# Performance work log

Measured on AMD Instinct MI355X. Metric: run time of the kernel, lower is better.

Reference implementation:

```python
import jax, jax.numpy as jnp
import numpy as np

D, E, N, DD, K = 1024, 2048, 16, 64, 4  # d_model, d_inner, d_state, dt_rank, d_conv
B, L = 2, 1024
EPS = 1e-5


def setup_inputs() -> dict:
    key = jax.random.key(0)
    ks = jax.random.split(key, 12)
    f = lambda k, s, scale=0.02: (jax.random.normal(k, s, jnp.float32) * scale)
    return dict(
        resid=jax.random.normal(ks[0], (B, L, D), jnp.float32),
        workplace_h=jnp.zeros((B, E, N), jnp.float32),
        norm_w=jnp.ones((D,), jnp.float32),
        skip_w=f(ks[1], (E, D)),
        in_w=f(ks[2], (E, D)),
        conv_w=f(ks[3], (E, 1, K), 0.2),
        conv_b=jnp.zeros((E,), jnp.float32),
        wd1=f(ks[4], (DD, E)),
        wd2_w=f(ks[5], (E, DD)),
        wd2_b=jnp.zeros((E,), jnp.float32),
        wb=f(ks[6], (N, E)),
        wc=f(ks[7], (N, E)),
        A_log=f(ks[8], (E, N), 1.0),
        W_D=jnp.ones((E,), jnp.float32),
        out_w=f(ks[9], (D, E)),
    )


def reference(resid, workplace_h, norm_w, skip_w, in_w, conv_w, conv_b,
              wd1, wd2_w, wd2_b, wb, wc, A_log, W_D, out_w):
    # RMSNorm
    x = resid * jax.lax.rsqrt(jnp.mean(resid ** 2, -1, keepdims=True) + EPS) * norm_w
    skip = x @ skip_w.T                      # [B,L,E]
    xi = x @ in_w.T                          # [B,L,E]
    # depthwise causal conv1d (torch pads both sides then slices to L; equivalent to left-pad K-1)
    xc = jnp.swapaxes(xi, 1, 2)              # [B,E,L]
    xc = jax.lax.conv_general_dilated(
        xc, conv_w, window_strides=(1,), padding=[(K - 1, 0)],
        feature_group_count=E, dimension_numbers=('NCH', 'OIH', 'NCH'))
    xc = xc + conv_b[None, :, None]
    x2 = jax.nn.silu(jnp.swapaxes(xc, 1, 2))  # [B,L,E]

    A = -jnp.exp(A_log)                       # [E,N]
    delta = jax.nn.softplus((x2 @ wd1.T) @ wd2_w.T + wd2_b)   # [B,L,E]
    A_bar = jnp.exp(delta[..., None] * A)                      # [B,L,E,N]
    Bm = x2 @ wb.T                                             # [B,L,N]
    B_bar = delta[..., None] * Bm[:, :, None, :]               # [B,L,E,N]
    Cm = x2 @ wc.T                                             # [B,L,N]

    def step(h, inp):
        a, b_, xl, cl = inp                   # [B,E,N],[B,E,N],[B,E],[B,N]
        h = a * h + b_ * xl[..., None]
        y = jnp.einsum('ben,bn->be', h, cl)
        return h, y

    h0 = jnp.zeros_like(workplace_h)          # workplace_h is zeroed (h[:] = 0)
    xs = (jnp.swapaxes(A_bar, 0, 1), jnp.swapaxes(B_bar, 0, 1),
          jnp.swapaxes(x2, 0, 1), jnp.swapaxes(Cm, 0, 1))
    _, ys = jax.lax.scan(step, h0, xs)        # ys: [L,B,E]
    y = jnp.swapaxes(ys, 0, 1)                # [B,L,E]

    y = (y + x2 * W_D) * jax.nn.silu(skip)
    return resid + y @ out_w.T
```

## Files before the change

kernel.cpp:

```cpp
#include <hip/hip_runtime.h>
#include <math.h>

#define Dm 1024
#define Em 2048
#define Nm 16
#define DDm 64
#define Bb 2
#define Lm 1024
#define Mrows (Bb*Lm)
#define NCH 32
#define CLEN 32
#define KS 16
#define KSO 4
#define PREPB 26112

typedef __attribute__((ext_vector_type(8))) short bf16x8;
typedef __attribute__((ext_vector_type(4))) float f32x4;
typedef unsigned int u32;
typedef unsigned short u16;

__device__ __forceinline__ u16 f2bf(float f) {
    union { float f; u32 u; } v; v.f = f;
    u32 r = v.u + 0x7fffu + ((v.u >> 16) & 1u);
    return (u16)(r >> 16);
}
__device__ __forceinline__ float bf2f(u16 v) {
    union { u32 u; float f; } t; t.u = ((u32)v) << 16; return t.f;
}

__device__ __forceinline__ void async_copy16(const void* g, void* l) {
    __builtin_amdgcn_global_load_lds(
        (const __attribute__((address_space(1))) u32*)g,
        (__attribute__((address_space(3))) u32*)l,
        16, 0, 0);
}

__global__ __launch_bounds__(256) void prep_rms_kernel(const float* __restrict__ skip_w,
                                                       const float* __restrict__ in_w,
                                                       const float* __restrict__ out_w,
                                                       const float* __restrict__ wd2_w,
                                                       const float* __restrict__ wb,
                                                       const float* __restrict__ wc,
                                                       const float* __restrict__ wd1,
                                                       const float* __restrict__ resid,
                                                       const float* __restrict__ norm_w,
                                                       u16* __restrict__ skip_w_bf,
                                                       u16* __restrict__ in_w_bf,
                                                       u16* __restrict__ out_w_bf,
                                                       u16* __restrict__ wd2_bf,
                                                       u16* __restrict__ wtb,
                                                       u16* __restrict__ x) {
    if (blockIdx.x < PREPB) {
        const int R0 = 2097152, R1 = 4194304, R2 = 6291456, R3 = 6422528, R4 = 6684672;
        int i = blockIdx.x * 256 + threadIdx.x;
        if (i < R0) skip_w_bf[i] = f2bf(skip_w[i]);
        else if (i < R1) in_w_bf[i - R0] = f2bf(in_w[i - R0]);
        else if (i < R2) out_w_bf[i - R1] = f2bf(out_w[i - R1]);
        else if (i < R3) wd2_bf[i - R2] = f2bf(wd2_w[i - R2]);
        else if (i < R4) {
            int j = i - R3;
            int c = j >> 11, k = j & 2047;
            float v = 0.f;
            if (c < 16) v = wb[(size_t)c * Em + k];
            else if (c < 32) v = wc[(size_t)(c - 16) * Em + k];
            else if (c < 96) v = wd1[(size_t)(c - 32) * Em + k];
            wtb[j] = f2bf(v);
        }
        return;
    }
    int row = blockIdx.x - PREPB;
    const float* r = resid + (size_t)row * Dm;
    float s = 0.f;
    for (int i = threadIdx.x; i < Dm; i += 256) { float v = r[i]; s += v * v; }
    __shared__ float red[4];
    for (int off = 32; off; off >>= 1) s += __shfl_down(s, off, 64);
    if ((threadIdx.x & 63) == 0) red[threadIdx.x >> 6] = s;
    __syncthreads();
    if (threadIdx.x == 0) {
        float t = red[0] + red[1] + red[2] + red[3];
        red[0] = rsqrtf(t / (float)Dm + 1e-5f);
    }
    __syncthreads();
    float sc = red[0];
    u16* xo = x + (size_t)row * Dm;
    for (int i = threadIdx.x; i < Dm; i += 256) xo[i] = f2bf(r[i] * sc * norm_w[i]);
}


__global__ __launch_bounds__(256) void gemm_db(const u16* __restrict__ A,
                                               const u16* __restrict__ W,
                                               const float* __restrict__ bias,
                                               float* __restrict__ C,
                                               float* __restrict__ C2, int split,
                                               int M, int N, int lda, int klen, int act) {
    __shared__ __align__(16) u16 As[2][128 * 32];
    __shared__ __align__(16) u16 Ws[2][64 * 32];
    int tid = threadIdx.x;
    int lane = tid & 63, wave = tid >> 6;
    int bm = blockIdx.y * 128, bn = blockIdx.x * 64;
    int kbase = blockIdx.z * klen;
    int lm = lane & 15, lq = lane >> 4;
    int wm = (wave & 1) * 64, wn = (wave >> 1) * 32;

    f32x4 acc[4][2] = {};
    int ldrow = lane >> 2;
    int gchunk = ((lane & 3) ^ ((lane >> 3) & 3)) * 8;
    int rdoff = (lq ^ ((lm >> 1) & 3)) * 8;

    const u16* Arow0 = A + (size_t)(bm + wave * 16 + ldrow) * lda + gchunk;
    const u16* Arow1 = A + (size_t)(bm + 64 + wave * 16 + ldrow) * lda + gchunk;
    const u16* Wrow  = W + (size_t)(bn + wave * 16 + ldrow) * lda + gchunk;
    int ldsA = (wave * 16) * 32;
    int ldsA2 = (64 + wave * 16) * 32;

    int nIter = klen / 32;
    async_copy16(Arow0 + kbase, &As[0][ldsA]);
    async_copy16(Arow1 + kbase, &As[0][ldsA2]);
    async_copy16(Wrow + kbase, &Ws[0][ldsA]);
    __syncthreads();

    for (int it = 0; it < nIter; ++it) {
        int cur = it & 1, nxt = cur ^ 1;
        if (it + 1 < nIter) {
            int k0 = kbase + (it + 1) * 32;
            async_copy16(Arow0 + k0, &As[nxt][ldsA]);
            async_copy16(Arow1 + k0, &As[nxt][ldsA2]);
            async_copy16(Wrow + k0, &Ws[nxt][ldsA]);
        }
        bf16x8 a[4], b[2];
        #pragma unroll
        for (int mi = 0; mi < 4; ++mi)
            a[mi] = *(const bf16x8*)&As[cur][(wm + mi * 16 + lm) * 32 + rdoff];
        #pragma unroll
        for (int nj = 0; nj < 2; ++nj)
            b[nj] = *(const bf16x8*)&Ws[cur][(wn + nj * 16 + lm) * 32 + rdoff];
        #pragma unroll
        for (int mi = 0; mi < 4; ++mi)
            #pragma unroll
            for (int nj = 0; nj < 2; ++nj)
                acc[mi][nj] = __builtin_amdgcn_mfma_f32_16x16x32_bf16(a[mi], b[nj], acc[mi][nj], 0, 0, 0);
        __syncthreads();
    }

    int ldc = C2 ? split : N;
    size_t zoff = (size_t)blockIdx.z * M * ldc;
    #pragma unroll
    for (int nj = 0; nj < 2; ++nj) {
        int col = bn + wn + nj * 16 + lm;
        float bv = bias ? bias[col] : 0.f;
        float* Cp = C; int colw = col;
        if (C2 && col >= split) { Cp = C2; colw = col - split; }
        #pragma unroll
        for (int mi = 0; mi < 4; ++mi) {
            #pragma unroll
            for (int r = 0; r < 4; ++r) {
                int row = bm + wm + mi * 16 + lq * 4 + r;
                float v = acc[mi][nj][r] + bv;
                size_t off = zoff + (size_t)row * ldc + colw;
                if (act == 1) {
                    v = fmaxf(v, 0.f) + __logf(1.f + __expf(-fabsf(v)));
                    Cp[off] = v;
                } else if (act == 2) {
                    ((u16*)Cp)[off] = f2bf(v);
                } else {
                    Cp[off] = v;
                }
            }
        }
    }
}

__global__ __launch_bounds__(256) void out_reduce_kernel(const float* __restrict__ part,
                                                         const float* __restrict__ resid,
                                                         float* __restrict__ out) {
    int idx = blockIdx.x * 256 + threadIdx.x;
    const float4* r4 = (const float4*)resid;
    const float4* p4 = (const float4*)part;
    float4 s = r4[idx];
    const int plane = Mrows * Dm / 4;
    #pragma unroll
    for (int ks = 0; ks < KSO; ++ks) {
        float4 p = p4[(size_t)ks * plane + idx];
        s.x += p.x; s.y += p.y; s.z += p.z; s.w += p.w;
    }
    ((float4*)out)[idx] = s;
}

__global__ __launch_bounds__(256) void small_reduce_kernel(const u16* __restrict__ Cp,
                                                           float* __restrict__ Bm,
                                                           float* __restrict__ Cm,
                                                           u16* __restrict__ d1) {
    int idx = blockIdx.x * 256 + threadIdx.x;
    int row = idx >> 7, col = idx & 127;
    float s = 0.f;
    #pragma unroll
    for (int ks = 0; ks < KS; ++ks) s += bf2f(Cp[(size_t)ks * (Mrows * 128) + idx]);
    if (col < 16) Bm[(size_t)row * 16 + col] = s;
    else if (col < 32) Cm[(size_t)row * 16 + (col - 16)] = s;
    else if (col < 96) d1[(size_t)row * 64 + (col - 32)] = f2bf(s);
}

__global__ __launch_bounds__(256) void conv_silu_kernel(const float* __restrict__ xi,
                                                        const float* __restrict__ cw,
                                                        const float* __restrict__ cb,
                                                        u16* __restrict__ x2b, int total) {
    int idx = blockIdx.x * 256 + threadIdx.x;
    if (idx >= total) return;
    int e = idx & (Em - 1);
    int l = (idx >> 11) & (Lm - 1);
    const float* base = xi + idx;
    float w0 = cw[e * 4 + 0], w1 = cw[e * 4 + 1], w2 = cw[e * 4 + 2], w3 = cw[e * 4 + 3];
    float acc = cb[e];
    if (l >= 3) acc += w0 * base[-3 * Em];
    if (l >= 2) acc += w1 * base[-2 * Em];
    if (l >= 1) acc += w2 * base[-1 * Em];
    acc += w3 * base[0];
    float v = acc / (1.f + __expf(-acc));
    x2b[idx] = f2bf(v);
}

__global__ __launch_bounds__(256) void scan1_kernel(const float* __restrict__ delta,
                                                    const u16* __restrict__ x2b,
                                                    const float* __restrict__ Bm,
                                                    const float* __restrict__ A_log,
                                                    float* __restrict__ h_end,
                                                    float* __restrict__ P) {
    int e = (blockIdx.x & 7) * 256 + threadIdx.x;
    int bc = blockIdx.x >> 3;
    int b = bc & 1, c = bc >> 1;
    float A[16];
    {
        const float4* al = (const float4*)(A_log + e * 16);
        float4 q0 = al[0], q1 = al[1], q2 = al[2], q3 = al[3];
        A[0]=-expf(q0.x); A[1]=-expf(q0.y); A[2]=-expf(q0.z); A[3]=-expf(q0.w);
        A[4]=-expf(q1.x); A[5]=-expf(q1.y); A[6]=-expf(q1.z); A[7]=-expf(q1.w);
        A[8]=-expf(q2.x); A[9]=-expf(q2.y); A[10]=-expf(q2.z); A[11]=-expf(q2.w);
        A[12]=-expf(q3.x); A[13]=-expf(q3.y); A[14]=-expf(q3.z); A[15]=-expf(q3.w);
    }
    float h[16], Pr[16];
    #pragma unroll
    for (int k = 0; k < 16; ++k) { h[k] = 0.f; Pr[k] = 1.f; }

    int l0 = c * CLEN;
    const float* dp = delta + ((size_t)(b * Lm + l0)) * Em + e;
    const u16* xp  = x2b   + ((size_t)(b * Lm + l0)) * Em + e;
    const float* bp = Bm    + ((size_t)(b * Lm + l0)) * Nm;

    float d_n = dp[0], x_n = bf2f(xp[0]);
    float4 b0n = *(const float4*)(bp + 0), b1n = *(const float4*)(bp + 4);
    float4 b2n = *(const float4*)(bp + 8), b3n = *(const float4*)(bp + 12);

    #pragma unroll 1
    for (int l = 0; l < CLEN; ++l) {
        float d = d_n, xv = x_n;
        float4 b0 = b0n, b1 = b1n, b2 = b2n, b3 = b3n;
        if (l < CLEN - 1) {
            d_n = dp[(size_t)(l + 1) * Em]; x_n = bf2f(xp[(size_t)(l + 1) * Em]);
            const float* nb = bp + (size_t)(l + 1) * Nm;
            b0n = *(const float4*)(nb); b1n = *(const float4*)(nb + 4);
            b2n = *(const float4*)(nb + 8); b3n = *(const float4*)(nb + 12);
        }
        float dx = d * xv;
        float bb[16] = {b0.x,b0.y,b0.z,b0.w, b1.x,b1.y,b1.z,b1.w,
                        b2.x,b2.y,b2.z,b2.w, b3.x,b3.y,b3.z,b3.w};
        #pragma unroll
        for (int k = 0; k < 16; ++k) {
            float a = __expf(d * A[k]);
            h[k] = a * h[k] + bb[k] * dx;
            Pr[k] *= a;
        }
    }
    size_t base = (((size_t)c * 2 + b) * 16) * 2048 + e;
    #pragma unroll
    for (int k = 0; k < 16; ++k) {
        h_end[base + k * 2048] = h[k];
        P[base + k * 2048] = Pr[k];
    }
}

__global__ __launch_bounds__(256) void scan2_kernel(float* __restrict__ h_end,
                                                    const float* __restrict__ P) {
    int T = blockIdx.x * 256 + threadIdx.x;
    float hi = 0.f;
    float he_n = h_end[T], p_n = P[T];
    #pragma unroll 1
    for (int c = 0; c < NCH; ++c) {
        float he = he_n, p = p_n;
        if (c < NCH - 1) {
            he_n = h_end[(size_t)(c + 1) * 65536 + T];
            p_n  = P[(size_t)(c + 1) * 65536 + T];
        }
        float hnew = fmaf(p, hi, he);
        h_end[(size_t)c * 65536 + T] = hi;
        hi = hnew;
    }
}

__global__ __launch_bounds__(256) void scan3_kernel(const float* __restrict__ delta,
                                                    const u16* __restrict__ x2b,
                                                    const float* __restrict__ Bm,
                                                    const float* __restrict__ Cm,
                                                    const float* __restrict__ A_log,
                                                    const float* __restrict__ h_init,
                                                    const float* __restrict__ skip,
                                                    const float* __restrict__ W_D,
                                                    u16* __restrict__ yb) {
    int e = (blockIdx.x & 7) * 256 + threadIdx.x;
    int bc = blockIdx.x >> 3;
    int b = bc & 1, c = bc >> 1;
    float A[16];
    {
        const float4* al = (const float4*)(A_log + e * 16);
        float4 q0 = al[0], q1 = al[1], q2 = al[2], q3 = al[3];
        A[0]=-expf(q0.x); A[1]=-expf(q0.y); A[2]=-expf(q0.z); A[3]=-expf(q0.w);
        A[4]=-expf(q1.x); A[5]=-expf(q1.y); A[6]=-expf(q1.z); A[7]=-expf(q1.w);
        A[8]=-expf(q2.x); A[9]=-expf(q2.y); A[10]=-expf(q2.z); A[11]=-expf(q2.w);
        A[12]=-expf(q3.x); A[13]=-expf(q3.y); A[14]=-expf(q3.z); A[15]=-expf(q3.w);
    }
    float h[16];
    {
        size_t base = (((size_t)c * 2 + b) * 16) * 2048 + e;
        #pragma unroll
        for (int k = 0; k < 16; ++k) h[k] = h_init[base + k * 2048];
    }
    float wd = W_D[e];

    int l0 = c * CLEN;
    const float* dp = delta + ((size_t)(b * Lm + l0)) * Em + e;
    const u16* xp  = x2b   + ((size_t)(b * Lm + l0)) * Em + e;
    const float* sp = skip  + ((size_t)(b * Lm + l0)) * Em + e;
    const float* bp = Bm    + ((size_t)(b * Lm + l0)) * Nm;
    const float* cp = Cm    + ((size_t)(b * Lm + l0)) * Nm;
    u16* yp = yb + ((size_t)(b * Lm + l0)) * Em + e;

    float d_n = dp[0], x_n = bf2f(xp[0]), s_n = sp[0];
    float4 b0n = *(const float4*)(bp + 0), b1n = *(const float4*)(bp + 4);
    float4 b2n = *(const float4*)(bp + 8), b3n = *(const float4*)(bp + 12);
    float4 c0n = *(const float4*)(cp + 0), c1n = *(const float4*)(cp + 4);
    float4 c2n = *(const float4*)(cp + 8), c3n = *(const float4*)(cp + 12);

    #pragma unroll 1
    for (int l = 0; l < CLEN; ++l) {
        float d = d_n, xv = x_n, sv = s_n;
        float4 b0 = b0n, b1 = b1n, b2 = b2n, b3 = b3n;
        float4 c0 = c0n, c1 = c1n, c2 = c2n, c3 = c3n;
        if (l < CLEN - 1) {
            d_n = dp[(size_t)(l + 1) * Em]; x_n = bf2f(xp[(size_t)(l + 1) * Em]);
            s_n = sp[(size_t)(l + 1) * Em];
            const float* nb = bp + (size_t)(l + 1) * Nm;
            b0n = *(const float4*)(nb); b1n = *(const float4*)(nb + 4);
            b2n = *(const float4*)(nb + 8); b3n = *(const float4*)(nb + 12);
            const float* nc = cp + (size_t)(l + 1) * Nm;
            c0n = *(const float4*)(nc); c1n = *(const float4*)(nc + 4);
            c2n = *(const float4*)(nc + 8); c3n = *(const float4*)(nc + 12);
        }
        float dx = d * xv;
        float bb[16] = {b0.x,b0.y,b0.z,b0.w, b1.x,b1.y,b1.z,b1.w,
                        b2.x,b2.y,b2.z,b2.w, b3.x,b3.y,b3.z,b3.w};
        float cc[16] = {c0.x,c0.y,c0.z,c0.w, c1.x,c1.y,c1.z,c1.w,
                        c2.x,c2.y,c2.z,c2.w, c3.x,c3.y,c3.z,c3.w};
        float yv = 0.f;
        #pragma unroll
        for (int k = 0; k < 16; ++k) {
            float a = __expf(d * A[k]);
            h[k] = a * h[k] + bb[k] * dx;
            yv += h[k] * cc[k];
        }
        float sig = 1.f / (1.f + __expf(-sv));
        yp[(size_t)l * Em] = f2bf((yv + xv * wd) * (sv * sig));
    }
}

extern "C" void kernel_launch(void* const* d_in, const int* in_sizes, int n_in,
                              void* d_out, int out_size, void* d_ws, size_t ws_size,
                              hipStream_t stream) {
    const float* resid  = (const float*)d_in[0];
    const float* norm_w = (const float*)d_in[2];
    const float* skip_w = (const float*)d_in[3];
    const float* in_w   = (const float*)d_in[4];
    const float* conv_w = (const float*)d_in[5];
    const float* conv_b = (const float*)d_in[6];
    const float* wd1    = (const float*)d_in[7];
    const float* wd2_w  = (const float*)d_in[8];
    const float* wd2_b  = (const float*)d_in[9];
    const float* wb     = (const float*)d_in[10];
    const float* wc     = (const float*)d_in[11];
    const float* A_log  = (const float*)d_in[12];
    const float* W_D    = (const float*)d_in[13];
    const float* out_w  = (const float*)d_in[14];
    float* out = (float*)d_out;

    float* ws = (float*)d_ws;
    float* region0 = ws; ws += 3 * 1024 * 1024;
    u16* x_bf      = (u16*)region0;
    u16* skip_w_bf = (u16*)(region0 + 1024 * 1024);
    u16* in_w_bf   = (u16*)(region0 + 2 * 1024 * 1024);
    float* h_endb  = region0;
    u16* out_w_bf  = (u16*)ws; ws += 1024 * 1024;
    u16* wd2_bf    = (u16*)ws; ws += 65536;
    u16* d1_bf     = (u16*)ws; ws += 65536;
    u16* wtb       = (u16*)ws; ws += 131072;
    float* Pbuf    = ws; ws += 2 * 1024 * 1024;
    u16* Cpart16   = (u16*)ws; ws += (size_t)KS * Mrows * 128 / 2;
    float* skip    = ws; ws += (size_t)Mrows * Em;
    float* xi      = ws; ws += (size_t)Mrows * Em;
    u16* x2_bf     = (u16*)ws; ws += (size_t)Mrows * Em / 2;
    u16* yb_bf     = (u16*)ws; ws += (size_t)Mrows * Em / 2;
    float* Bmb     = ws; ws += (size_t)Mrows * Nm;
    float* Cmb     = ws; ws += (size_t)Mrows * Nm;
    float* delta   = xi;
    float* OutPart = skip;

    const int M = Mrows;

    prep_rms_kernel<<<PREPB + M, 256, 0, stream>>>(
        skip_w, in_w, out_w, wd2_w, wb, wc, wd1, resid, norm_w,
        skip_w_bf, in_w_bf, out_w_bf, wd2_bf, wtb, x_bf);

    gemm_db<<<dim3(2 * Em / 64, M / 128, 1), 256, 0, stream>>>(
        x_bf, skip_w_bf, nullptr, skip, xi, Em, M, 2 * Em, Dm, Dm, 0);

    conv_silu_kernel<<<(M * Em) / 256, 256, 0, stream>>>(xi, conv_w, conv_b, x2_bf, M * Em);

    gemm_db<<<dim3(128 / 64, M / 128, KS), 256, 0, stream>>>(
        x2_bf, wtb, nullptr, (float*)Cpart16, nullptr, 0, M, 128, Em, Em / KS, 2);
    small_reduce_kernel<<<(M * 128) / 256, 256, 0, stream>>>(Cpart16, Bmb, Cmb, d1_bf);

    gemm_db<<<dim3(Em / 64, M / 128, 1), 256, 0, stream>>>(
        d1_bf, wd2_bf, wd2_b, delta, nullptr, 0, M, Em, DDm, DDm, 1);

    scan1_kernel<<<Bb * NCH * 8, 256, 0, stream>>>(delta, x2_bf, Bmb, A_log, h_endb, Pbuf);
    scan2_kernel<<<65536 / 256, 256, 0, stream>>>(h_endb, Pbuf);
    scan3_kernel<<<Bb * NCH * 8, 256, 0, stream>>>(delta, x2_bf, Bmb, Cmb, A_log, h_endb,
                                                   skip, W_D, yb_bf);

    gemm_db<<<dim3(Dm / 64, M / 128, KSO), 256, 0, stream>>>(
        yb_bf, out_w_bf, nullptr, OutPart, nullptr, 0, M, Dm, Em, Em / KSO, 0);
    out_reduce_kernel<<<(M * Dm / 4) / 256, 256, 0, stream>>>(OutPart, resid, out);
}
```

Measured before the change: 275.0 us.

## Store intermediates in bf16 and add a single-shot small-K GEMM kernel

Switches the skip, xi, delta and out-projection partial-sum buffers from fp32 to bf16, which roughly halves global memory traffic for conv, scan and reduce stages. Adds gemm_smallk, which loads the whole short K range into LDS with async copies and does no double buffering; it serves the B/C/dt projection and the dt-up projection with fused softplus. The cost is lower precision, notably bf16 delta and bf16 split-K partial sums before the final residual add, plus a larger static LDS footprint in the new kernel.

```diff
diff --git a/kernel.cpp b/kernel.cpp
--- a/kernel.cpp
+++ b/kernel.cpp
@@ -157,31 +157,91 @@
                 int row = bm + wm + mi * 16 + lq * 4 + r;
                 float v = acc[mi][nj][r] + bv;
                 size_t off = zoff + (size_t)row * ldc + colw;
-                if (act == 1) {
+                if (act == 2) ((u16*)Cp)[off] = f2bf(v);
+                else Cp[off] = v;
+            }
+        }
+    }
+}
+
+__global__ __launch_bounds__(256) void gemm_smallk(const u16* __restrict__ A,
+                                                   const u16* __restrict__ W,
+                                                   const float* __restrict__ bias,
+                                                   u16* __restrict__ C,
+                                                   int M, int N, int lda, int klen, int act) {
+    __shared__ __align__(16) u16 As[4][128 * 32];
+    __shared__ __align__(16) u16 Ws[4][64 * 32];
+    int tid = threadIdx.x;
+    int lane = tid & 63, wave = tid >> 6;
+    int bm = blockIdx.y * 128, bn = blockIdx.x * 64;
+    int kbase = blockIdx.z * klen;
+    int lm = lane & 15, lq = lane >> 4;
+    int wm = (wave & 1) * 64, wn = (wave >> 1) * 32;
+
+    f32x4 acc[4][2] = {};
+    int ldrow = lane >> 2;
+    int gchunk = ((lane & 3) ^ ((lane >> 3) & 3)) * 8;
+    int rdoff = (lq ^ ((lm >> 1) & 3)) * 8;
+
+    const u16* Arow0 = A + (size_t)(bm + wave * 16 + ldrow) * lda + gchunk;
+    const u16* Arow1 = A + (size_t)(bm + 64 + wave * 16 + ldrow) * lda + gchunk;
+    const u16* Wrow  = W + (size_t)(bn + wave * 16 + ldrow) * lda + gchunk;
+    int ldsA = (wave * 16) * 32;
+    int ldsA2 = (64 + wave * 16) * 32;
+
+    int nIter = klen / 32;
+    for (int it = 0; it < nIter; ++it) {
+        int k0 = kbase + it * 32;
+        async_copy16(Arow0 + k0, &As[it][ldsA]);
+        async_copy16(Arow1 + k0, &As[it][ldsA2]);
+        async_copy16(Wrow + k0, &Ws[it][ldsA]);
+    }
+    __syncthreads();
+
+    for (int it = 0; it < nIter; ++it) {
+        bf16x8 a[4], b[2];
+        #pragma unroll
+        for (int mi = 0; mi < 4; ++mi)
+            a[mi] = *(const bf16x8*)&As[it][(wm + mi * 16 + lm) * 32 + rdoff];
+        #pragma unroll
+        for (int nj = 0; nj < 2; ++nj)
+            b[nj] = *(const bf16x8*)&Ws[it][(wn + nj * 16 + lm) * 32 + rdoff];
+        #pragma unroll
+        for (int mi = 0; mi < 4; ++mi)
+            #pragma unroll
+            for (int nj = 0; nj < 2; ++nj)
+                acc[mi][nj] = __builtin_amdgcn_mfma_f32_16x16x32_bf16(a[mi], b[nj], acc[mi][nj], 0, 0, 0);
+    }
+
+    size_t zoff = (size_t)blockIdx.z * M * N;
+    #pragma unroll
+    for (int nj = 0; nj < 2; ++nj) {
+        int col = bn + wn + nj * 16 + lm;
+        float bv = bias ? bias[col] : 0.f;
+        #pragma unroll
+        for (int mi = 0; mi < 4; ++mi) {
+            #pragma unroll
+            for (int r = 0; r < 4; ++r) {
+                int row = bm + wm + mi * 16 + lq * 4 + r;
+                float v = acc[mi][nj][r] + bv;
+                if (act == 1)
                     v = fmaxf(v, 0.f) + __logf(1.f + __expf(-fabsf(v)));
-                    Cp[off] = v;
-                } else if (act == 2) {
-                    ((u16*)Cp)[off] = f2bf(v);
-                } else {
-                    Cp[off] = v;
-                }
+                C[zoff + (size_t)row * N + col] = f2bf(v);
             }
         }
     }
 }
 
-__global__ __launch_bounds__(256) void out_reduce_kernel(const float* __restrict__ part,
+__global__ __launch_bounds__(256) void out_reduce_kernel(const u16* __restrict__ part,
                                                          const float* __restrict__ resid,
                                                          float* __restrict__ out) {
     int idx = blockIdx.x * 256 + threadIdx.x;
-    const float4* r4 = (const float4*)resid;
-    const float4* p4 = (const float4*)part;
-    float4 s = r4[idx];
-    const int plane = Mrows * Dm / 4;
+    float4 s = ((const float4*)resid)[idx];
+    const int planeQ = Mrows * Dm / 4;
     #pragma unroll
     for (int ks = 0; ks < KSO; ++ks) {
-        float4 p = p4[(size_t)ks * plane + idx];
-        s.x += p.x; s.y += p.y; s.z += p.z; s.w += p.w;
+        ushort4 p = ((const ushort4*)part)[(size_t)ks * planeQ + idx];
+        s.x += bf2f(p.x); s.y += bf2f(p.y); s.z += bf2f(p.z); s.w += bf2f(p.w);
     }
     ((float4*)out)[idx] = s;
 }
@@ -200,7 +260,7 @@
     else if (col < 96) d1[(size_t)row * 64 + (col - 32)] = f2bf(s);
 }
 
-__global__ __launch_bounds__(256) void conv_silu_kernel(const float* __restrict__ xi,
+__global__ __launch_bounds__(256) void conv_silu_kernel(const u16* __restrict__ xi,
                                                         const float* __restrict__ cw,
                                                         const float* __restrict__ cb,
                                                         u16* __restrict__ x2b, int total) {
@@ -208,18 +268,18 @@
     if (idx >= total) return;
     int e = idx & (Em - 1);
     int l = (idx >> 11) & (Lm - 1);
-    const float* base = xi + idx;
+    const u16* base = xi + idx;
     float w0 = cw[e * 4 + 0], w1 = cw[e * 4 + 1], w2 = cw[e * 4 + 2], w3 = cw[e * 4 + 3];
     float acc = cb[e];
-    if (l >= 3) acc += w0 * base[-3 * Em];
-    if (l >= 2) acc += w1 * base[-2 * Em];
-    if (l >= 1) acc += w2 * base[-1 * Em];
-    acc += w3 * base[0];
+    if (l >= 3) acc += w0 * bf2f(base[-3 * Em]);
+    if (l >= 2) acc += w1 * bf2f(base[-2 * Em]);
+    if (l >= 1) acc += w2 * bf2f(base[-1 * Em]);
+    acc += w3 * bf2f(base[0]);
     float v = acc / (1.f + __expf(-acc));
     x2b[idx] = f2bf(v);
 }
 
-__global__ __launch_bounds__(256) void scan1_kernel(const float* __restrict__ delta,
+__global__ __launch_bounds__(256) void scan1_kernel(const u16* __restrict__ delta,
                                                     const u16* __restrict__ x2b,
                                                     const float* __restrict__ Bm,
                                                     const float* __restrict__ A_log,
@@ -242,11 +302,11 @@
     for (int k = 0; k < 16; ++k) { h[k] = 0.f; Pr[k] = 1.f; }
 
     int l0 = c * CLEN;
-    const float* dp = delta + ((size_t)(b * Lm + l0)) * Em + e;
+    const u16* dp  = delta + ((size_t)(b * Lm + l0)) * Em + e;
     const u16* xp  = x2b   + ((size_t)(b * Lm + l0)) * Em + e;
-    const float* bp = Bm    + ((size_t)(b * Lm + l0)) * Nm;
-
-    float d_n = dp[0], x_n = bf2f(xp[0]);
+    const float* bp = Bm   + ((size_t)(b * Lm + l0)) * Nm;
+
+    float d_n = bf2f(dp[0]), x_n = bf2f(xp[0]);
     float4 b0n = *(const float4*)(bp + 0), b1n = *(const float4*)(bp + 4);
     float4 b2n = *(const float4*)(bp + 8), b3n = *(const float4*)(bp + 12);
 
@@ -255,7 +315,7 @@
         float d = d_n, xv = x_n;
         float4 b0 = b0n, b1 = b1n, b2 = b2n, b3 = b3n;
         if (l < CLEN - 1) {
-            d_n = dp[(size_t)(l + 1) * Em]; x_n = bf2f(xp[(size_t)(l + 1) * Em]);
+            d_n = bf2f(dp[(size_t)(l + 1) * Em]); x_n = bf2f(xp[(size_t)(l + 1) * Em]);
             const float* nb = bp + (size_t)(l + 1) * Nm;
             b0n = *(const float4*)(nb); b1n = *(const float4*)(nb + 4);
             b2n = *(const float4*)(nb + 8); b3n = *(const float4*)(nb + 12);
@@ -296,13 +356,13 @@
     }
 }
 
-__global__ __launch_bounds__(256) void scan3_kernel(const float* __restrict__ delta,
+__global__ __launch_bounds__(256) void scan3_kernel(const u16* __restrict__ delta,
                                                     const u16* __restrict__ x2b,
                                                     const float* __restrict__ Bm,
                                                     const float* __restrict__ Cm,
                                                     const float* __restrict__ A_log,
                                                     const float* __restrict__ h_init,
-                                                    const float* __restrict__ skip,
+                                                    const u16* __restrict__ skip,
                                                     const float* __restrict__ W_D,
                                                     u16* __restrict__ yb) {
     int e = (blockIdx.x & 7) * 256 + threadIdx.x;
@@ -326,14 +386,14 @@
     float wd = W_D[e];
 
     int l0 = c * CLEN;
-    const float* dp = delta + ((size_t)(b * Lm + l0)) * Em + e;
+    const u16* dp  = delta + ((size_t)(b * Lm + l0)) * Em + e;
     const u16* xp  = x2b   + ((size_t)(b * Lm + l0)) * Em + e;
-    const float* sp = skip  + ((size_t)(b * Lm + l0)) * Em + e;
-    const float* bp = Bm    + ((size_t)(b * Lm + l0)) * Nm;
-    const float* cp = Cm    + ((size_t)(b * Lm + l0)) * Nm;
+    const u16* sp  = skip  + ((size_t)(b * Lm + l0)) * Em + e;
+    const float* bp = Bm   + ((size_t)(b * Lm + l0)) * Nm;
+    const float* cp = Cm   + ((size_t)(b * Lm + l0)) * Nm;
     u16* yp = yb + ((size_t)(b * Lm + l0)) * Em + e;
 
-    float d_n = dp[0], x_n = bf2f(xp[0]), s_n = sp[0];
+    float d_n = bf2f(dp[0]), x_n = bf2f(xp[0]), s_n = bf2f(sp[0]);
     float4 b0n = *(const float4*)(bp + 0), b1n = *(const float4*)(bp + 4);
     float4 b2n = *(const float4*)(bp + 8), b3n = *(const float4*)(bp + 12);
     float4 c0n = *(const float4*)(cp + 0), c1n = *(const float4*)(cp + 4);
@@ -345,8 +405,8 @@
         float4 b0 = b0n, b1 = b1n, b2 = b2n, b3 = b3n;
         float4 c0 = c0n, c1 = c1n, c2 = c2n, c3 = c3n;
         if (l < CLEN - 1) {
-            d_n = dp[(size_t)(l + 1) * Em]; x_n = bf2f(xp[(size_t)(l + 1) * Em]);
-            s_n = sp[(size_t)(l + 1) * Em];
+            d_n = bf2f(dp[(size_t)(l + 1) * Em]); x_n = bf2f(xp[(size_t)(l + 1) * Em]);
+            s_n = bf2f(sp[(size_t)(l + 1) * Em]);
             const float* nb = bp + (size_t)(l + 1) * Nm;
             b0n = *(const float4*)(nb); b1n = *(const float4*)(nb + 4);
             b2n = *(const float4*)(nb + 8); b3n = *(const float4*)(nb + 12);
@@ -402,14 +462,14 @@
     u16* wtb       = (u16*)ws; ws += 131072;
     float* Pbuf    = ws; ws += 2 * 1024 * 1024;
     u16* Cpart16   = (u16*)ws; ws += (size_t)KS * Mrows * 128 / 2;
-    float* skip    = ws; ws += (size_t)Mrows * Em;
-    float* xi      = ws; ws += (size_t)Mrows * Em;
+    u16* skip_bf   = (u16*)ws; ws += (size_t)Mrows * Em / 2;
+    u16* xi_bf     = (u16*)ws; ws += (size_t)Mrows * Em / 2;
     u16* x2_bf     = (u16*)ws; ws += (size_t)Mrows * Em / 2;
     u16* yb_bf     = (u16*)ws; ws += (size_t)Mrows * Em / 2;
+    u16* OutPart16 = (u16*)ws; ws += (size_t)KSO * Mrows * Dm / 2;
     float* Bmb     = ws; ws += (size_t)Mrows * Nm;
     float* Cmb     = ws; ws += (size_t)Mrows * Nm;
-    float* delta   = xi;
-    float* OutPart = skip;
+    u16* delta16   = xi_bf;
 
     const int M = Mrows;
 
@@ -418,23 +478,23 @@
         skip_w_bf, in_w_bf, out_w_bf, wd2_bf, wtb, x_bf);
 
     gemm_db<<<dim3(2 * Em / 64, M / 128, 1), 256, 0, stream>>>(
-        x_bf, skip_w_bf, nullptr, skip, xi, Em, M, 2 * Em, Dm, Dm, 0);
-
-    conv_silu_kernel<<<(M * Em) / 256, 256, 0, stream>>>(xi, conv_w, conv_b, x2_bf, M * Em);
-
-    gemm_db<<<dim3(128 / 64, M / 128, KS), 256, 0, stream>>>(
-        x2_bf, wtb, nullptr, (float*)Cpart16, nullptr, 0, M, 128, Em, Em / KS, 2);
+        x_bf, skip_w_bf, nullptr, (float*)skip_bf, (float*)xi_bf, Em, M, 2 * Em, Dm, Dm, 2);
+
+    conv_silu_kernel<<<(M * Em) / 256, 256, 0, stream>>>(xi_bf, conv_w, conv_b, x2_bf, M * Em);
+
+    gemm_smallk<<<dim3(128 / 64, M / 128, KS), 256, 0, stream>>>(
+        x2_bf, wtb, nullptr, Cpart16, M, 128, Em, Em / KS, 0);
     small_reduce_kernel<<<(M * 128) / 256, 256, 0, stream>>>(Cpart16, Bmb, Cmb, d1_bf);
 
-    gemm_db<<<dim3(Em / 64, M / 128, 1), 256, 0, stream>>>(
-        d1_bf, wd2_bf, wd2_b, delta, nullptr, 0, M, Em, DDm, DDm, 1);
-
-    scan1_kernel<<<Bb * NCH * 8, 256, 0, stream>>>(delta, x2_bf, Bmb, A_log, h_endb, Pbuf);
+    gemm_smallk<<<dim3(Em / 64, M / 128, 1), 256, 0, stream>>>(
+        d1_bf, wd2_bf, wd2_b, delta16, M, Em, DDm, DDm, 1);
+
+    scan1_kernel<<<Bb * NCH * 8, 256, 0, stream>>>(delta16, x2_bf, Bmb, A_log, h_endb, Pbuf);
     scan2_kernel<<<65536 / 256, 256, 0, stream>>>(h_endb, Pbuf);
-    scan3_kernel<<<Bb * NCH * 8, 256, 0, stream>>>(delta, x2_bf, Bmb, Cmb, A_log, h_endb,
-                                                   skip, W_D, yb_bf);
+    scan3_kernel<<<Bb * NCH * 8, 256, 0, stream>>>(delta16, x2_bf, Bmb, Cmb, A_log, h_endb,
+                                                   skip_bf, W_D, yb_bf);
 
     gemm_db<<<dim3(Dm / 64, M / 128, KSO), 256, 0, stream>>>(
-        yb_bf, out_w_bf, nullptr, OutPart, nullptr, 0, M, Dm, Em, Em / KSO, 0);
-    out_reduce_kernel<<<(M * Dm / 4) / 256, 256, 0, stream>>>(OutPart, resid, out);
-}
+        yb_bf, out_w_bf, nullptr, (float*)OutPart16, nullptr, 0, M, Dm, Em, Em / KSO, 2);
+    out_reduce_kernel<<<(M * Dm / 4) / 256, 256, 0, stream>>>(OutPart16, resid, out);
+}
```

Result: faster. 261.2 us (-5.0%).
